# Performance work log

Hardware: AMD Instinct MI355X
Metric: run time of the kernel (lower is better)

Reference implementation:

```python
import jax, jax.numpy as jnp
import numpy as np

B, S, W, D, H = 2, 2048, 32, 1024, 16

def setup_inputs() -> dict:
    key = jax.random.key(0)
    ks = jax.random.split(key, 8)
    scale = 0.02
    return {
        'q': jax.random.normal(ks[0], (B, S, D), jnp.float32),
        'k': jax.random.normal(ks[1], (B, S, W, D), jnp.float32),
        'v': jax.random.normal(ks[2], (B, S, W, D), jnp.float32),
        'Wq': jax.random.normal(ks[3], (D, D), jnp.float32) * scale,
        'bq': jnp.zeros((D,), jnp.float32),
        'Wk': jax.random.normal(ks[4], (D, D), jnp.float32) * scale,
        'bk': jnp.zeros((D,), jnp.float32),
        'Wv': jax.random.normal(ks[5], (D, D), jnp.float32) * scale,
        'bv': jnp.zeros((D,), jnp.float32),
        'Wo': jax.random.normal(ks[6], (D, D), jnp.float32) * scale,
        'bo': jnp.zeros((D,), jnp.float32),
        'num_heads': H,
    }

def reference(q, k, v, Wq, bq, Wk, bk, Wv, bv, Wo, bo, num_heads):
    b, s, d = q.shape
    w = k.shape[2]
    hd = d // num_heads
    # query: Linear -> view(B,S,H,1,hd) -> transpose(1,2) => (B,H,S,1,hd)
    qh = (q @ Wq.T + bq).reshape(b, s, num_heads, 1, hd).transpose(0, 2, 1, 3, 4)
    # key/value: Linear then RAW view (B,H,S,W,hd) -- faithful to torch .view (no head transpose)
    kh = (k @ Wk.T + bk).reshape(b, num_heads, s, w, hd)
    vh = (v @ Wv.T + bv).reshape(b, num_heads, s, w, hd)
    # scores: (B,H,S,1,W), scaled by sqrt(head_dim) (query.shape[-1] inside attention)
    scores = jnp.einsum('bhsid,bhswd->bhsiw', qh, kh) / jnp.sqrt(jnp.float32(hd))
    # Softmax(dim=1) normalizes over the HEAD axis -- faithful to the original
    attn = jax.nn.softmax(scores, axis=1)
    A = jnp.einsum('bhsiw,bhswd->bhsid', attn, vh)[:, :, :, 0, :]  # (B,H,S,hd)
    out = A.reshape(b, s, d)  # raw view, matches torch .view(B,S,D)
    return out @ Wo.T + bo
```

## Files before the change

### kernel.cpp

```cpp
#include <hip/hip_runtime.h>
#include <hip/hip_bf16.h>


#define DEVI __device__ __forceinline__

typedef __attribute__((ext_vector_type(8))) short bf16x8;
typedef __attribute__((ext_vector_type(4))) float f32x4;
typedef const __attribute__((address_space(1))) void* gvp;
typedef __attribute__((address_space(3))) void* lvp;

DEVI ushort f2bf(float f) {
  uint u = __float_as_uint(f);
  u = u + 0x7fffu + ((u >> 16) & 1u);
  return (ushort)(u >> 16);
}
DEVI float bf2f(ushort u) { return __uint_as_float(((uint)u) << 16); }

__global__ __launch_bounds__(256) void cast_kernel(const float* __restrict__ in,
                                                   ushort* __restrict__ out,
                                                   long n) {
  long i = ((long)blockIdx.x * 256 + threadIdx.x) * 8;
  const long stride = (long)gridDim.x * 256 * 8;
  for (; i < n; i += stride) {
    float4 a = *reinterpret_cast<const float4*>(in + i);
    float4 b = *reinterpret_cast<const float4*>(in + i + 4);
    ushort o[8];
    o[0] = f2bf(a.x); o[1] = f2bf(a.y); o[2] = f2bf(a.z); o[3] = f2bf(a.w);
    o[4] = f2bf(b.x); o[5] = f2bf(b.y); o[6] = f2bf(b.z); o[7] = f2bf(b.w);
    *reinterpret_cast<int4*>(out + i) = *reinterpret_cast<const int4*>(o);
  }
}

template <int FI0, int FJ0>
DEVI void mfma16(f32x4 (&acc)[8][4], const bf16x8 (&A)[4][2],
                 const bf16x8 (&B)[2][2]) {
  __builtin_amdgcn_s_setprio(1);
#pragma unroll
  for (int i = 0; i < 4; ++i)
#pragma unroll
    for (int j = 0; j < 2; ++j)
#pragma unroll
      for (int kk = 0; kk < 2; ++kk)
        acc[FI0 + i][FJ0 + j] = __builtin_amdgcn_mfma_f32_16x16x32_bf16(
            A[i][kk], B[j][kk], acc[FI0 + i][FJ0 + j], 0, 0, 0);
  __builtin_amdgcn_s_setprio(0);
}

__global__ __launch_bounds__(512, 2) void gemm_big(const ushort* __restrict__ Ag,
                                                   const ushort* __restrict__ Wg,
                                                   const float* __restrict__ bias,
                                                   ushort* __restrict__ Cg) {
  constexpr int K = 1024;
  __shared__ char lds[131072];
  const int tid = threadIdx.x;
  const int lane = tid & 63;
  const int wave = tid >> 6;
  const int wm = wave >> 2;
  const int wn = wave & 3;
  const int d = blockIdx.x;
  const int bn = (d >> 3) & 3;
  const size_t bm = (size_t)(d & 7) * (gridDim.x >> 5) + (d >> 5);

  const ushort* aB = Ag + bm * 256 * K;
  const ushort* bB = Wg + (size_t)bn * 256 * K;

  const int r0 = tid >> 3;
  const int c0 = (tid & 7) ^ (r0 & 7);
  const ushort* aS0 = aB + (size_t)r0 * K + c0 * 8;
  const ushort* aS1 = aB + (size_t)(r0 + 64) * K + c0 * 8;
  const ushort* aS2 = aB + (size_t)(r0 + 128) * K + c0 * 8;
  const ushort* aS3 = aB + (size_t)(r0 + 192) * K + c0 * 8;
  const ushort* bS0 = bB + (size_t)r0 * K + c0 * 8;
  const ushort* bS1 = bB + (size_t)(r0 + 64) * K + c0 * 8;
  const ushort* bS2 = bB + (size_t)(r0 + 128) * K + c0 * 8;
  const ushort* bS3 = bB + (size_t)(r0 + 192) * K + c0 * 8;
  const int dst0 = tid * 16;
  const int dst1 = tid * 16 + 8192;

  const int lm = lane & 15;
  const int q = lane >> 4;
  const int rowB = lm * 128;
  const int swz0 = (q ^ (lm & 7)) * 16;
  const int swz1 = ((4 + q) ^ (lm & 7)) * 16;
  const char* ldsc = (const char*)lds;
  const char* p0A = ldsc + wm * 16384 + rowB;
  const char* p0B = ldsc + 32768 + (wn >> 1) * 16384 + (wn & 1) * 8192 + rowB;
  const char* p1A = p0A + 65536;
  const char* p1B = p0B + 65536;

  f32x4 acc[8][4] = {};
  bf16x8 aF[4][2], aG[4][2], bF[2][2], bG[2][2];

#define STG(p0, p1, kb, ldsOff)                                                  \
  {                                                                              \
    __builtin_amdgcn_global_load_lds((gvp)((p0) + (kb)),                         \
                                     (lvp)(lds + (ldsOff) + dst0), 16, 0, 0);    \
    __builtin_amdgcn_global_load_lds((gvp)((p1) + (kb)),                         \
                                     (lvp)(lds + (ldsOff) + dst1), 16, 0, 0);    \
  }
#define PH_SYNC()                                    \
  __builtin_amdgcn_s_barrier();                      \
  asm volatile("s_waitcnt lgkmcnt(0)" ::: "memory"); \
  __builtin_amdgcn_sched_barrier(0);
#define LDA(dst, p)                                                          \
  _Pragma("unroll") for (int i_ = 0; i_ < 4; ++i_) {                         \
    dst[i_][0] = *reinterpret_cast<const bf16x8*>((p) + i_ * 2048 + swz0);   \
    dst[i_][1] = *reinterpret_cast<const bf16x8*>((p) + i_ * 2048 + swz1);   \
  }
#define LDB(dst, p)                                                          \
  _Pragma("unroll") for (int j_ = 0; j_ < 2; ++j_) {                         \
    dst[j_][0] = *reinterpret_cast<const bf16x8*>((p) + j_ * 2048 + swz0);   \
    dst[j_][1] = *reinterpret_cast<const bf16x8*>((p) + j_ * 2048 + swz1);   \
  }

  STG(aS0, aS1, 0, 0);
  STG(aS2, aS3, 0, 16384);
  STG(bS0, bS1, 0, 32768);
  STG(bS2, bS3, 0, 49152);
  STG(aS0, aS1, 64, 65536);
  STG(aS2, aS3, 64, 65536 + 16384);
  __builtin_amdgcn_sched_barrier(0);
  asm volatile("s_waitcnt vmcnt(4)" ::: "memory");
  __builtin_amdgcn_s_barrier();
  __builtin_amdgcn_sched_barrier(0);

  for (int it = 0; it < 8; ++it) {
    const int kb1 = it * 128 + 64;
    const int kb2 = it * 128 + 128;
    const int kb3 = it * 128 + 192;
    const bool pf = (it < 7);

    LDA(aF, p0A);
    LDB(bF, p0B);
    STG(bS0, bS1, kb1, 65536 + 32768);
    PH_SYNC();
    mfma16<0, 0>(acc, aF, bF);
    __builtin_amdgcn_s_barrier();

    LDA(aG, p0A + 8192);
    STG(bS2, bS3, kb1, 65536 + 49152);
    PH_SYNC();
    mfma16<4, 0>(acc, aG, bF);
    __builtin_amdgcn_s_barrier();

    LDB(bG, p0B + 4096);
    if (pf) STG(aS0, aS1, kb2, 0);
    PH_SYNC();
    mfma16<0, 2>(acc, aF, bG);
    __builtin_amdgcn_s_barrier();

    if (pf) STG(aS2, aS3, kb2, 16384);
    PH_SYNC();
    mfma16<4, 2>(acc, aG, bG);
    __builtin_amdgcn_sched_barrier(0);
    if (pf)
      asm volatile("s_waitcnt vmcnt(4)" ::: "memory");
    else
      asm volatile("s_waitcnt vmcnt(0)" ::: "memory");
    __builtin_amdgcn_s_barrier();
    __builtin_amdgcn_sched_barrier(0);

    LDA(aF, p1A);
    LDB(bF, p1B);
    if (pf) STG(bS0, bS1, kb2, 32768);
    PH_SYNC();
    mfma16<0, 0>(acc, aF, bF);
    __builtin_amdgcn_s_barrier();

    LDA(aG, p1A + 8192);
    if (pf) STG(bS2, bS3, kb2, 49152);
    PH_SYNC();
    mfma16<4, 0>(acc, aG, bF);
    __builtin_amdgcn_s_barrier();

    LDB(bG, p1B + 4096);
    if (pf) STG(aS0, aS1, kb3, 65536);
    PH_SYNC();
    mfma16<0, 2>(acc, aF, bG);
    __builtin_amdgcn_s_barrier();

    if (pf) STG(aS2, aS3, kb3, 65536 + 16384);
    PH_SYNC();
    mfma16<4, 2>(acc, aG, bG);
    if (it < 7) {
      __builtin_amdgcn_sched_barrier(0);
      asm volatile("s_waitcnt vmcnt(4)" ::: "memory");
      __builtin_amdgcn_s_barrier();
      __builtin_amdgcn_sched_barrier(0);
    }
  }
#undef STG
#undef PH_SYNC
#undef LDA
#undef LDB

#pragma unroll
  for (int fi = 0; fi < 8; ++fi) {
#pragma unroll
    for (int fj = 0; fj < 4; ++fj) {
      int n = bn * 256 + wn * 64 + fj * 16 + lm;
      float bv = bias[n];
#pragma unroll
      for (int r = 0; r < 4; ++r) {
        size_t m = bm * 256 + wm * 128 + fi * 16 + ((lane >> 4) * 4) + r;
        Cg[m * 1024 + n] = f2bf(acc[fi][fj][r] + bv);
      }
    }
  }
}

template <typename TOUT>
__global__ __launch_bounds__(256) void gemm_lds(const ushort* __restrict__ Ag,
                                                const ushort* __restrict__ Wg,
                                                const float* __restrict__ bias,
                                                TOUT* __restrict__ Cg) {
  constexpr int K = 1024;
  __shared__ ushort lA[128 * 64];
  __shared__ ushort lB[128 * 64];
  const int tid = threadIdx.x;
  const int lane = tid & 63;
  const int wave = tid >> 6;
  const int wr = (wave >> 1) * 64;
  const int wc = (wave & 1) * 64;
  const int d = blockIdx.x;
  const int bn = (d >> 3) & 7;
  const size_t bm = (size_t)(d & 7) * (gridDim.x >> 6) + (d >> 6);

  const ushort* aB = Ag + bm * 128 * K;
  const ushort* bB = Wg + (size_t)bn * 128 * K;
  const int srow = wave * 32 + (lane >> 3);
  const int scol = ((lane & 7) ^ (lane >> 3)) * 8;
  char* lAc = (char*)lA;
  char* lBc = (char*)lB;

  f32x4 acc[4][4] = {};

  for (int kt = 0; kt < K; kt += 64) {
    __syncthreads();
#pragma unroll
    for (int c = 0; c < 4; ++c) {
      __builtin_amdgcn_global_load_lds(
          (gvp)(aB + (size_t)(srow + c * 8) * K + kt + scol),
          (lvp)(lAc + wave * 4096 + c * 1024), 16, 0, 0);
      __builtin_amdgcn_global_load_lds(
          (gvp)(bB + (size_t)(srow + c * 8) * K + kt + scol),
          (lvp)(lBc + wave * 4096 + c * 1024), 16, 0, 0);
    }
    __syncthreads();
#pragma unroll
    for (int kk = 0; kk < 2; ++kk) {
      bf16x8 af[4], bg[4];
#pragma unroll
      for (int fi = 0; fi < 4; ++fi) {
        int r = wr + fi * 16 + (lane & 15);
        int byte = (r * 128 + kk * 64 + ((lane >> 4) * 16)) ^ ((r & 7) << 4);
        af[fi] = *reinterpret_cast<const bf16x8*>(lAc + byte);
      }
#pragma unroll
      for (int fj = 0; fj < 4; ++fj) {
        int r = wc + fj * 16 + (lane & 15);
        int byte = (r * 128 + kk * 64 + ((lane >> 4) * 16)) ^ ((r & 7) << 4);
        bg[fj] = *reinterpret_cast<const bf16x8*>(lBc + byte);
      }
#pragma unroll
      for (int fi = 0; fi < 4; ++fi)
#pragma unroll
        for (int fj = 0; fj < 4; ++fj)
          acc[fi][fj] = __builtin_amdgcn_mfma_f32_16x16x32_bf16(af[fi], bg[fj],
                                                                acc[fi][fj], 0, 0, 0);
    }
  }
#pragma unroll
  for (int fi = 0; fi < 4; ++fi) {
#pragma unroll
    for (int fj = 0; fj < 4; ++fj) {
      int n = bn * 128 + wc + fj * 16 + (lane & 15);
      float bv = bias[n];
#pragma unroll
      for (int r = 0; r < 4; ++r) {
        size_t m = bm * 128 + wr + fi * 16 + ((lane >> 4) * 4) + r;
        float val = acc[fi][fj][r] + bv;
        if constexpr (sizeof(TOUT) == 2)
          reinterpret_cast<ushort*>(Cg)[m * 1024 + n] = f2bf(val);
        else
          reinterpret_cast<float*>(Cg)[m * 1024 + n] = val;
      }
    }
  }
}

template <typename TIN, typename TOUT>
__global__ __launch_bounds__(256) void gemm_bias(const TIN* __restrict__ Ag,
                                                 const float* __restrict__ Wg,
                                                 const float* __restrict__ bias,
                                                 TOUT* __restrict__ Cg) {
  constexpr int K = 1024;
  __shared__ char lA[128 * 64 * 2];
  __shared__ char lB[128 * 64 * 2];
  const int tid = threadIdx.x;
  const int lane = tid & 63;
  const int wave = tid >> 6;
  const int wr = (wave >> 1) * 64;
  const int wc = (wave & 1) * 64;
  const int bn = blockIdx.x;
  const size_t bm = blockIdx.y;

  const TIN* aBase = Ag + bm * 128 * K;
  const float* bBase = Wg + (size_t)bn * 128 * K;

  f32x4 acc[4][4] = {};

  for (int kt = 0; kt < K; kt += 64) {
    __syncthreads();
    if constexpr (sizeof(TIN) == 4) {
#pragma unroll
      for (int i = 0; i < 8; ++i) {
        int f = tid + i * 256;
        int row = f >> 4, c4 = f & 15;
        const float4 v = *reinterpret_cast<const float4*>(
            reinterpret_cast<const float*>(aBase) + (size_t)row * K + kt + c4 * 4);
        ushort4 pk;
        pk.x = f2bf(v.x); pk.y = f2bf(v.y); pk.z = f2bf(v.z); pk.w = f2bf(v.w);
        int byte = (row * 128 + c4 * 8) ^ ((row & 7) << 4);
        *reinterpret_cast<ushort4*>(lA + byte) = pk;
      }
    } else {
#pragma unroll
      for (int i = 0; i < 4; ++i) {
        int f = tid + i * 256;
        int row = f >> 3, c8 = f & 7;
        int4 v = *reinterpret_cast<const int4*>(
            reinterpret_cast<const ushort*>(aBase) + (size_t)row * K + kt + c8 * 8);
        int byte = (row * 128 + c8 * 16) ^ ((row & 7) << 4);
        *reinterpret_cast<int4*>(lA + byte) = v;
      }
    }
#pragma unroll
    for (int i = 0; i < 8; ++i) {
      int f = tid + i * 256;
      int row = f >> 4, c4 = f & 15;
      const float4 v =
          *reinterpret_cast<const float4*>(bBase + (size_t)row * K + kt + c4 * 4);
      ushort4 pk;
      pk.x = f2bf(v.x); pk.y = f2bf(v.y); pk.z = f2bf(v.z); pk.w = f2bf(v.w);
      int byte = (row * 128 + c4 * 8) ^ ((row & 7) << 4);
      *reinterpret_cast<ushort4*>(lB + byte) = pk;
    }
    __syncthreads();
#pragma unroll
    for (int kk = 0; kk < 2; ++kk) {
      bf16x8 af[4], bg[4];
#pragma unroll
      for (int fi = 0; fi < 4; ++fi) {
        int r = wr + fi * 16 + (lane & 15);
        int byte = (r * 128 + kk * 64 + ((lane >> 4) * 16)) ^ ((r & 7) << 4);
        af[fi] = *reinterpret_cast<const bf16x8*>(lA + byte);
      }
#pragma unroll
      for (int fj = 0; fj < 4; ++fj) {
        int r = wc + fj * 16 + (lane & 15);
        int byte = (r * 128 + kk * 64 + ((lane >> 4) * 16)) ^ ((r & 7) << 4);
        bg[fj] = *reinterpret_cast<const bf16x8*>(lB + byte);
      }
#pragma unroll
      for (int fi = 0; fi < 4; ++fi)
#pragma unroll
        for (int fj = 0; fj < 4; ++fj)
          acc[fi][fj] =
              __builtin_amdgcn_mfma_f32_16x16x32_bf16(af[fi], bg[fj], acc[fi][fj], 0, 0, 0);
    }
  }
#pragma unroll
  for (int fi = 0; fi < 4; ++fi) {
#pragma unroll
    for (int fj = 0; fj < 4; ++fj) {
      int n = bn * 128 + wc + fj * 16 + (lane & 15);
      float bv = bias[n];
#pragma unroll
      for (int r = 0; r < 4; ++r) {
        size_t m = bm * 128 + wr + fi * 16 + ((lane >> 4) * 4) + r;
        float val = acc[fi][fj][r] + bv;
        if constexpr (sizeof(TOUT) == 2)
          reinterpret_cast<ushort*>(Cg)[m * 1024 + n] = f2bf(val);
        else
          reinterpret_cast<float*>(Cg)[m * 1024 + n] = val;
      }
    }
  }
}

__global__ __launch_bounds__(512) void attn_kernel(const ushort* __restrict__ Q,
                                                   const ushort* __restrict__ Kl,
                                                   const ushort* __restrict__ Vl,
                                                   ushort* __restrict__ Aout) {
  const int bs = blockIdx.x;
  const int b = bs >> 11, sp = bs & 2047;
  const int tid = threadIdx.x;
  const int wave = tid >> 6, lane = tid & 63;

  __shared__ ushort qrow[1024];
  __shared__ float sc[16][32];
  __shared__ float attnw[16][32];
  __shared__ float mx[32], rinv[32];

  reinterpret_cast<uint*>(qrow)[tid] =
      reinterpret_cast<const uint*>(Q + (size_t)bs * 1024)[tid];
  __syncthreads();

  const int wp = lane & 31, half = lane >> 5;
#pragma unroll
  for (int hh = 0; hh < 2; ++hh) {
    const int h = wave * 2 + hh;
    const int s_k = h * 128 + (sp >> 4);
    const int w_k = (sp & 15) * 2 + (wp >> 4);
    const ushort* kp =
        Kl + (((size_t)(b * 2048 + s_k) * 32) + w_k) * 1024 + (wp & 15) * 64 + half * 32;
    const ushort* qp = qrow + h * 64 + half * 32;
    float dot = 0.f;
#pragma unroll
    for (int j = 0; j < 32; j += 8) {
      int4 kv = *reinterpret_cast<const int4*>(kp + j);
      int4 qv = *reinterpret_cast<const int4*>(qp + j);
      const ushort* ka = reinterpret_cast<const ushort*>(&kv);
      const ushort* qa = reinterpret_cast<const ushort*>(&qv);
#pragma unroll
      for (int t = 0; t < 8; ++t) dot += bf2f(ka[t]) * bf2f(qa[t]);
    }
    dot += __shfl_xor(dot, 32);
    if (half == 0) sc[h][wp] = dot * 0.125f;
  }
  __syncthreads();
  if (tid < 32) {
    float m = sc[0][tid];
#pragma unroll
    for (int h = 1; h < 16; ++h) m = fmaxf(m, sc[h][tid]);
    float s = 0.f;
#pragma unroll
    for (int h = 0; h < 16; ++h) s += __expf(sc[h][tid] - m);
    mx[tid] = m;
    rinv[tid] = 1.f / s;
  }
  __syncthreads();
  if (lane < 32) {
#pragma unroll
    for (int hh = 0; hh < 2; ++hh) {
      const int h = wave * 2 + hh;
      attnw[h][lane] = __expf(sc[h][lane] - mx[lane]) * rinv[lane];
    }
  }
  __syncthreads();
#pragma unroll
  for (int hh = 0; hh < 2; ++hh) {
    const int h = wave * 2 + hh;
    const int s_k = h * 128 + (sp >> 4);
    const size_t vb = (((size_t)(b * 2048 + s_k) * 32) + (sp & 15) * 2) * 1024;
    float a = 0.f;
#pragma unroll
    for (int w2 = 0; w2 < 32; ++w2) {
      float wgt = attnw[h][w2];
      a += wgt * bf2f(Vl[vb + (size_t)(w2 >> 4) * 1024 + (w2 & 15) * 64 + lane]);
    }
    Aout[(((size_t)(b * 16 + h)) * 2048 + sp) * 64 + lane] = f2bf(a);
  }
}

extern "C" void kernel_launch(void* const* d_in, const int* in_sizes, int n_in,
                              void* d_out, int out_size, void* d_ws, size_t ws_size,
                              hipStream_t stream) {
  const float* q = (const float*)d_in[0];
  const float* k = (const float*)d_in[1];
  const float* v = (const float*)d_in[2];
  const float* Wq = (const float*)d_in[3];
  const float* bq = (const float*)d_in[4];
  const float* Wk = (const float*)d_in[5];
  const float* bk = (const float*)d_in[6];
  const float* Wv = (const float*)d_in[7];
  const float* bv = (const float*)d_in[8];
  const float* Wo = (const float*)d_in[9];
  const float* bo = (const float*)d_in[10];
  float* out = (float*)d_out;

  char* ws = (char*)d_ws;
  const size_t MB = 1u << 20;
  ushort* Qlin = (ushort*)ws;
  ushort* Aws  = (ushort*)(ws + 8 * MB);
  ushort* wkbf = (ushort*)(ws + 16 * MB);
  ushort* wvbf = (ushort*)(ws + 18 * MB);
  ushort* wqbf = (ushort*)(ws + 20 * MB);
  ushort* wobf = (ushort*)(ws + 22 * MB);
  ushort* qbf  = (ushort*)(ws + 24 * MB);
  ushort* Klin = (ushort*)(ws + 32 * MB);
  ushort* Vlin = (ushort*)(ws + 288 * MB);
  ushort* kvbf = (ushort*)(ws + 544 * MB);
  const bool full = ws_size >= 800 * MB;

  const long NKV = 134217728L;

  if (full) {
    cast_kernel<<<dim3(512), 256, 0, stream>>>(Wq, wqbf, 1048576L);
    cast_kernel<<<dim3(512), 256, 0, stream>>>(Wk, wkbf, 1048576L);
    cast_kernel<<<dim3(512), 256, 0, stream>>>(Wv, wvbf, 1048576L);
    cast_kernel<<<dim3(512), 256, 0, stream>>>(Wo, wobf, 1048576L);
    cast_kernel<<<dim3(2048), 256, 0, stream>>>(q, qbf, 4194304L);
    gemm_lds<ushort><<<dim3(256), 256, 0, stream>>>(qbf, wqbf, bq, Qlin);
    cast_kernel<<<dim3(4096), 256, 0, stream>>>(k, kvbf, NKV);
    gemm_big<<<dim3(2048), 512, 0, stream>>>(kvbf, wkbf, bk, Klin);
    cast_kernel<<<dim3(4096), 256, 0, stream>>>(v, kvbf, NKV);
    gemm_big<<<dim3(2048), 512, 0, stream>>>(kvbf, wvbf, bv, Vlin);
    attn_kernel<<<dim3(4096), dim3(512), 0, stream>>>(Qlin, Klin, Vlin, Aws);
    gemm_lds<float><<<dim3(256), 256, 0, stream>>>(Aws, wobf, bo, out);
  } else {
    gemm_bias<float, ushort><<<dim3(8, 32), 256, 0, stream>>>(q, Wq, bq, Qlin);
    gemm_bias<float, ushort><<<dim3(8, 1024), 256, 0, stream>>>(k, Wk, bk, Klin);
    gemm_bias<float, ushort><<<dim3(8, 1024), 256, 0, stream>>>(v, Wv, bv, Vlin);
    attn_kernel<<<dim3(4096), dim3(512), 0, stream>>>(Qlin, Klin, Vlin, Aws);
    gemm_bias<ushort, float><<<dim3(8, 32), 256, 0, stream>>>(Aws, Wo, bo, out);
  }
}
```

Before: 1.049 ms.

## Fuse fp32-to-bf16 cast of K/V inputs into the projection GEMM loads

The K and V projection GEMM now reads fp32 activations directly into registers, converts them to bf16 with packed convert instructions, and writes them to swizzled LDS. This replaces the direct global-to-LDS loads of a pre-cast bf16 buffer. The separate cast kernels and the intermediate bf16 workspace are removed, eliminating a full write and re-read of the K/V tensors. In exchange, the main loop is restructured with register staging, new wait-count tuning and peeled tail iterations. This raises register pressure and adds VALU and LDS-store work inside the pipelined loop.

```diff
diff --git a/kernel.cpp b/kernel.cpp
--- a/kernel.cpp
+++ b/kernel.cpp
@@ -46,7 +46,7 @@
   __builtin_amdgcn_s_setprio(0);
 }
 
-__global__ __launch_bounds__(512, 2) void gemm_big(const ushort* __restrict__ Ag,
+__global__ __launch_bounds__(512, 2) void gemm_big(const float* __restrict__ Ag,
                                                    const ushort* __restrict__ Wg,
                                                    const float* __restrict__ bias,
                                                    ushort* __restrict__ Cg) {
@@ -61,21 +61,16 @@
   const int bn = (d >> 3) & 3;
   const size_t bm = (size_t)(d & 7) * (gridDim.x >> 5) + (d >> 5);
 
-  const ushort* aB = Ag + bm * 256 * K;
   const ushort* bB = Wg + (size_t)bn * 256 * K;
 
   const int r0 = tid >> 3;
   const int c0 = (tid & 7) ^ (r0 & 7);
-  const ushort* aS0 = aB + (size_t)r0 * K + c0 * 8;
-  const ushort* aS1 = aB + (size_t)(r0 + 64) * K + c0 * 8;
-  const ushort* aS2 = aB + (size_t)(r0 + 128) * K + c0 * 8;
-  const ushort* aS3 = aB + (size_t)(r0 + 192) * K + c0 * 8;
+  const float* pR0 = Ag + bm * 256 * K + (size_t)r0 * K + c0 * 8;
+  const float* pR1 = pR0 + 64 * K;
   const ushort* bS0 = bB + (size_t)r0 * K + c0 * 8;
   const ushort* bS1 = bB + (size_t)(r0 + 64) * K + c0 * 8;
   const ushort* bS2 = bB + (size_t)(r0 + 128) * K + c0 * 8;
   const ushort* bS3 = bB + (size_t)(r0 + 192) * K + c0 * 8;
-  const int dst0 = tid * 16;
-  const int dst1 = tid * 16 + 8192;
 
   const int lm = lane & 15;
   const int q = lane >> 4;
@@ -90,18 +85,44 @@
 
   f32x4 acc[8][4] = {};
   bf16x8 aF[4][2], aG[4][2], bF[2][2], bG[2][2];
-
-#define STG(p0, p1, kb, ldsOff)                                                  \
+  float4 sa[4], sb[4], sc[4], sd[4];
+
+#define SB0 __builtin_amdgcn_sched_barrier(0)
+#define STG(p0, p1, ktE, ldsOff)                                                 \
   {                                                                              \
-    __builtin_amdgcn_global_load_lds((gvp)((p0) + (kb)),                         \
-                                     (lvp)(lds + (ldsOff) + dst0), 16, 0, 0);    \
-    __builtin_amdgcn_global_load_lds((gvp)((p1) + (kb)),                         \
-                                     (lvp)(lds + (ldsOff) + dst1), 16, 0, 0);    \
+    __builtin_amdgcn_global_load_lds((gvp)((p0) + (ktE)),                        \
+                                     (lvp)(lds + (ldsOff) + tid * 16), 16, 0, 0);\
+    __builtin_amdgcn_global_load_lds((gvp)((p1) + (ktE)),                        \
+                                     (lvp)(lds + (ldsOff) + 8192 + tid * 16),    \
+                                     16, 0, 0);                                  \
+  }
+#define AISS(set, off)                                                \
+  {                                                                   \
+    set[0] = *reinterpret_cast<const float4*>(pR0 + (off));           \
+    set[1] = *reinterpret_cast<const float4*>(pR0 + (off) + 4);       \
+    set[2] = *reinterpret_cast<const float4*>(pR1 + (off));           \
+    set[3] = *reinterpret_cast<const float4*>(pR1 + (off) + 4);       \
+  }
+#define CVT(set, base)                                                          \
+  {                                                                             \
+    uint w0, w1, w2, w3;                                                        \
+    asm("v_cvt_pk_bf16_f32 %0,%1,%2" : "=v"(w0) : "v"(set[0].x), "v"(set[0].y));\
+    asm("v_cvt_pk_bf16_f32 %0,%1,%2" : "=v"(w1) : "v"(set[0].z), "v"(set[0].w));\
+    asm("v_cvt_pk_bf16_f32 %0,%1,%2" : "=v"(w2) : "v"(set[1].x), "v"(set[1].y));\
+    asm("v_cvt_pk_bf16_f32 %0,%1,%2" : "=v"(w3) : "v"(set[1].z), "v"(set[1].w));\
+    *reinterpret_cast<uint4*>(lds + (base) + tid * 16) =                        \
+        make_uint4(w0, w1, w2, w3);                                             \
+    asm("v_cvt_pk_bf16_f32 %0,%1,%2" : "=v"(w0) : "v"(set[2].x), "v"(set[2].y));\
+    asm("v_cvt_pk_bf16_f32 %0,%1,%2" : "=v"(w1) : "v"(set[2].z), "v"(set[2].w));\
+    asm("v_cvt_pk_bf16_f32 %0,%1,%2" : "=v"(w2) : "v"(set[3].x), "v"(set[3].y));\
+    asm("v_cvt_pk_bf16_f32 %0,%1,%2" : "=v"(w3) : "v"(set[3].z), "v"(set[3].w));\
+    *reinterpret_cast<uint4*>(lds + (base) + 8192 + tid * 16) =                 \
+        make_uint4(w0, w1, w2, w3);                                             \
   }
 #define PH_SYNC()                                    \
   __builtin_amdgcn_s_barrier();                      \
   asm volatile("s_waitcnt lgkmcnt(0)" ::: "memory"); \
-  __builtin_amdgcn_sched_barrier(0);
+  SB0;
 #define LDA(dst, p)                                                          \
   _Pragma("unroll") for (int i_ = 0; i_ < 4; ++i_) {                         \
     dst[i_][0] = *reinterpret_cast<const bf16x8*>((p) + i_ * 2048 + swz0);   \
@@ -113,86 +134,111 @@
     dst[j_][1] = *reinterpret_cast<const bf16x8*>((p) + j_ * 2048 + swz1);   \
   }
 
-  STG(aS0, aS1, 0, 0);
-  STG(aS2, aS3, 0, 16384);
-  STG(bS0, bS1, 0, 32768);
-  STG(bS2, bS3, 0, 49152);
-  STG(aS0, aS1, 64, 65536);
-  STG(aS2, aS3, 64, 65536 + 16384);
-  __builtin_amdgcn_sched_barrier(0);
-  asm volatile("s_waitcnt vmcnt(4)" ::: "memory");
+  AISS(sc, 0); SB0;
+  AISS(sd, 131072); SB0;
+  CVT(sc, 0); SB0;
+  CVT(sd, 16384); SB0;
+  AISS(sc, 64); SB0;
+  AISS(sd, 131072 + 64); SB0;
+  CVT(sc, 65536); SB0;
+  CVT(sd, 81920); SB0;
+  STG(bS0, bS1, 0, 32768); SB0;
+  AISS(sa, 128); SB0;
+  STG(bS2, bS3, 0, 49152); SB0;
+  AISS(sb, 131072 + 128); SB0;
+  asm volatile("s_waitcnt vmcnt(10)" ::: "memory");
+  asm volatile("s_waitcnt lgkmcnt(0)" ::: "memory");
   __builtin_amdgcn_s_barrier();
-  __builtin_amdgcn_sched_barrier(0);
-
-  for (int it = 0; it < 8; ++it) {
-    const int kb1 = it * 128 + 64;
-    const int kb2 = it * 128 + 128;
-    const int kb3 = it * 128 + 192;
-    const bool pf = (it < 7);
-
-    LDA(aF, p0A);
-    LDB(bF, p0B);
-    STG(bS0, bS1, kb1, 65536 + 32768);
-    PH_SYNC();
-    mfma16<0, 0>(acc, aF, bF);
-    __builtin_amdgcn_s_barrier();
-
-    LDA(aG, p0A + 8192);
-    STG(bS2, bS3, kb1, 65536 + 49152);
-    PH_SYNC();
-    mfma16<4, 0>(acc, aG, bF);
-    __builtin_amdgcn_s_barrier();
-
-    LDB(bG, p0B + 4096);
-    if (pf) STG(aS0, aS1, kb2, 0);
-    PH_SYNC();
-    mfma16<0, 2>(acc, aF, bG);
-    __builtin_amdgcn_s_barrier();
-
-    if (pf) STG(aS2, aS3, kb2, 16384);
-    PH_SYNC();
-    mfma16<4, 2>(acc, aG, bG);
-    __builtin_amdgcn_sched_barrier(0);
-    if (pf)
-      asm volatile("s_waitcnt vmcnt(4)" ::: "memory");
-    else
-      asm volatile("s_waitcnt vmcnt(0)" ::: "memory");
-    __builtin_amdgcn_s_barrier();
-    __builtin_amdgcn_sched_barrier(0);
-
-    LDA(aF, p1A);
-    LDB(bF, p1B);
-    if (pf) STG(bS0, bS1, kb2, 32768);
-    PH_SYNC();
-    mfma16<0, 0>(acc, aF, bF);
-    __builtin_amdgcn_s_barrier();
-
-    LDA(aG, p1A + 8192);
-    if (pf) STG(bS2, bS3, kb2, 49152);
-    PH_SYNC();
-    mfma16<4, 0>(acc, aG, bF);
-    __builtin_amdgcn_s_barrier();
-
-    LDB(bG, p1B + 4096);
-    if (pf) STG(aS0, aS1, kb3, 65536);
-    PH_SYNC();
-    mfma16<0, 2>(acc, aF, bG);
-    __builtin_amdgcn_s_barrier();
-
-    if (pf) STG(aS2, aS3, kb3, 65536 + 16384);
-    PH_SYNC();
-    mfma16<4, 2>(acc, aG, bG);
-    if (it < 7) {
-      __builtin_amdgcn_sched_barrier(0);
-      asm volatile("s_waitcnt vmcnt(4)" ::: "memory");
-      __builtin_amdgcn_s_barrier();
-      __builtin_amdgcn_sched_barrier(0);
-    }
-  }
+  SB0;
+
+#define ITER(M)                                                             \
+  {                                                                         \
+    const int ktB1 = (2 * it + 1) * 64;                                     \
+    const int ktB2 = (2 * it + 2) * 64;                                     \
+    const int offC = (2 * it + 3) * 64;                                     \
+    const int offA2 = (2 * it + 4) * 64;                                    \
+                                                                   \
+    LDA(aF, p0A); LDB(bF, p0B);                                             \
+    STG(bS0, bS1, ktB1, 98304);                                             \
+    PH_SYNC();                                                              \
+    mfma16<0, 0>(acc, aF, bF);                                              \
+    __builtin_amdgcn_s_barrier();                                           \
+                                                                   \
+    if (M < 2) AISS(sc, offC);                                              \
+    STG(bS2, bS3, ktB1, 114688);                                            \
+    LDA(aG, p0A + 8192);                                                    \
+    PH_SYNC();                                                              \
+    mfma16<4, 0>(acc, aG, bF);                                              \
+    SB0;                                                                    \
+    if (M < 2) { asm volatile("s_waitcnt vmcnt(12)" ::: "memory"); }        \
+    else       { asm volatile("s_waitcnt vmcnt(4)" ::: "memory"); }         \
+    __builtin_amdgcn_s_barrier();                                           \
+    SB0;                                                                    \
+                                                                   \
+    if (M < 2) { CVT(sa, 0); CVT(sb, 16384); AISS(sd, 131072 + offC); }     \
+    LDB(bG, p0B + 4096);                                                    \
+    PH_SYNC();                                                              \
+    mfma16<0, 2>(acc, aF, bG);                                              \
+    __builtin_amdgcn_s_barrier();                                           \
+                                                                   \
+    mfma16<4, 2>(acc, aG, bG);                                              \
+    SB0;                                                                    \
+    if (M < 2) { asm volatile("s_waitcnt vmcnt(10)" ::: "memory"); }        \
+    else       { asm volatile("s_waitcnt vmcnt(2)" ::: "memory"); }         \
+    __builtin_amdgcn_s_barrier();                                           \
+    SB0;                                                                    \
+                                                                   \
+    LDA(aF, p1A); LDB(bF, p1B);                                             \
+    if (M < 2) STG(bS0, bS1, ktB2, 32768);                                  \
+    PH_SYNC();                                                              \
+    mfma16<0, 0>(acc, aF, bF);                                              \
+    __builtin_amdgcn_s_barrier();                                           \
+                                                                   \
+    if (M == 0) AISS(sa, offA2);                                            \
+    if (M < 2) STG(bS2, bS3, ktB2, 49152);                                  \
+    LDA(aG, p1A + 8192);                                                    \
+    PH_SYNC();                                                              \
+    mfma16<4, 0>(acc, aG, bF);                                              \
+    SB0;                                                                    \
+    if (M == 0)      { asm volatile("s_waitcnt vmcnt(12)" ::: "memory"); }  \
+    else if (M == 1) { asm volatile("s_waitcnt vmcnt(8)" ::: "memory"); }   \
+    else             { asm volatile("s_waitcnt vmcnt(0)" ::: "memory"); }   \
+    __builtin_amdgcn_s_barrier();                                           \
+    SB0;                                                                    \
+                                                                   \
+    if (M < 2) { CVT(sc, 65536); CVT(sd, 81920); }                          \
+    if (M == 0) AISS(sb, 131072 + offA2);                                   \
+    LDB(bG, p1B + 4096);                                                    \
+    PH_SYNC();                                                              \
+    mfma16<0, 2>(acc, aF, bG);                                              \
+    __builtin_amdgcn_s_barrier();                                           \
+                                                                   \
+    mfma16<4, 2>(acc, aG, bG);                                              \
+    if (M == 0) {                                                           \
+      SB0;                                                                  \
+      asm volatile("s_waitcnt vmcnt(10)" ::: "memory");                     \
+      __builtin_amdgcn_s_barrier();                                         \
+      SB0;                                                                  \
+    } else if (M == 1) {                                                    \
+      SB0;                                                                  \
+      asm volatile("s_waitcnt vmcnt(2)" ::: "memory");                      \
+      __builtin_amdgcn_s_barrier();                                         \
+      SB0;                                                                  \
+    }                                                                       \
+  }
+
+#pragma unroll 1
+  for (int it = 0; it < 6; ++it) ITER(0);
+  { const int it = 6; ITER(1); }
+  { const int it = 7; ITER(2); }
+#undef ITER
 #undef STG
+#undef AISS
+#undef CVT
 #undef PH_SYNC
 #undef LDA
 #undef LDB
+#undef SB0
 
 #pragma unroll
   for (int fi = 0; fi < 8; ++fi) {
@@ -491,10 +537,7 @@
   ushort* qbf  = (ushort*)(ws + 24 * MB);
   ushort* Klin = (ushort*)(ws + 32 * MB);
   ushort* Vlin = (ushort*)(ws + 288 * MB);
-  ushort* kvbf = (ushort*)(ws + 544 * MB);
   const bool full = ws_size >= 800 * MB;
-
-  const long NKV = 134217728L;
 
   if (full) {
     cast_kernel<<<dim3(512), 256, 0, stream>>>(Wq, wqbf, 1048576L);
@@ -503,10 +546,8 @@
     cast_kernel<<<dim3(512), 256, 0, stream>>>(Wo, wobf, 1048576L);
     cast_kernel<<<dim3(2048), 256, 0, stream>>>(q, qbf, 4194304L);
     gemm_lds<ushort><<<dim3(256), 256, 0, stream>>>(qbf, wqbf, bq, Qlin);
-    cast_kernel<<<dim3(4096), 256, 0, stream>>>(k, kvbf, NKV);
-    gemm_big<<<dim3(2048), 512, 0, stream>>>(kvbf, wkbf, bk, Klin);
-    cast_kernel<<<dim3(4096), 256, 0, stream>>>(v, kvbf, NKV);
-    gemm_big<<<dim3(2048), 512, 0, stream>>>(kvbf, wvbf, bv, Vlin);
+    gemm_big<<<dim3(2048), 512, 0, stream>>>(k, wkbf, bk, Klin);
+    gemm_big<<<dim3(2048), 512, 0, stream>>>(v, wvbf, bv, Vlin);
     attn_kernel<<<dim3(4096), dim3(512), 0, stream>>>(Qlin, Klin, Vlin, Aws);
     gemm_lds<float><<<dim3(256), 256, 0, stream>>>(Aws, wobf, bo, out);
   } else {
```

Measured after the change: 2.273 ms. 117% more time.
